# Performance work log

Measured on AMD Instinct MI355X. Metric: run time of the kernel, lower is better.

Reference implementation:

```python
import jax, jax.numpy as jnp
import numpy as np

WET_MIX = 0.3
FEEDBACK = 0.4
ROOM_SIZE = 0.5
NUM_REFL = 8
NUM_HEADS = 4

# Delay kernel table: int(delay) in {0,1,2,>=3} -> kernel_size {identity,3,5,7}.
# A k-tap kernel with padding k//2 == the same kernel zero-padded to 7 taps with padding 3.
def _gauss7(ks):
    g = np.exp(-np.linspace(-2.0, 2.0, ks) ** 2)
    g = g / g.sum()
    out = np.zeros(7, np.float32)
    s = (7 - ks) // 2
    out[s:s + ks] = g
    return out
_delta = np.zeros(7, np.float32); _delta[3] = 1.0
K_TABLE = jnp.asarray(np.stack([_delta, _gauss7(3), _gauss7(5), _gauss7(7)]))  # [4,7]


def _conv2d(x, w, b, pad):
    y = jax.lax.conv_general_dilated(x, w, (1, 1), [(pad, pad), (pad, pad)],
                                     dimension_numbers=('NCHW', 'OIHW', 'NCHW'))
    return y + b[None, :, None, None]


def _delay_line(x, kern7):
    # vertical depthwise Gaussian blur, same for every (batch, channel) plane
    b, c, h, w = x.shape
    k = kern7.reshape(1, 1, 7, 1)
    y = jax.lax.conv_general_dilated(x.reshape(b * c, 1, h, w), k, (1, 1), [(3, 3), (0, 0)],
                                     dimension_numbers=('NCHW', 'OIHW', 'NCHW'))
    return y.reshape(b, c, h, w)


def _forward(x, refl_w, refl_d, sc_w, sc_b, fb_w, fb_b, d1_w, d1_b, d2_w, d2_b,
             in_proj_w, in_proj_b, out_proj_w, out_proj_b, oc_w, oc_b):
    B, C, H, W = x.shape
    scaled = refl_d * ROOM_SIZE
    kidx = jnp.clip(jnp.floor(scaled).astype(jnp.int32), 0, 3)  # int(delay) detaches grad, as in torch

    wet = jnp.zeros_like(x)
    fb_buf = x * 0.1
    spatial = _conv2d(x, sc_w, sc_b, 1)  # [B,2C,H,W]

    for i in range(NUM_REFL):
        refl = _delay_line(fb_buf, K_TABLE[kidx[i]])
        refl = _conv2d(refl, fb_w, fb_b, 1)
        damp = jax.nn.sigmoid(_conv2d(jax.nn.silu(_conv2d(refl, d1_w, d1_b, 0)), d2_w, d2_b, 0))
        refl = refl * damp
        weight = jax.nn.sigmoid(refl_w[i]) * (0.8 ** i)
        wet = wet + refl * weight
        fb_buf = fb_buf + refl * (FEEDBACK * 0.1)

    # MultiheadAttention over L = H*W tokens, embed_dim=C=4, 4 heads (head_dim=1)
    L = H * W
    hd = C // NUM_HEADS
    wet_flat = wet.reshape(B, C, L).transpose(0, 2, 1)           # [B,L,C]
    qkv = wet_flat @ in_proj_w.T + in_proj_b                     # [B,L,3C]
    q, k, v = jnp.split(qkv, 3, axis=-1)
    def heads(t):
        return t.reshape(B, L, NUM_HEADS, hd).transpose(0, 2, 1, 3)  # [B,H,L,hd]
    q, k, v = heads(q), heads(k), heads(v)
    scores = jnp.einsum('bhqd,bhkd->bhqk', q, k) / np.sqrt(hd).astype(np.float32)
    attn = jax.nn.softmax(scores, axis=-1)
    o = jnp.einsum('bhqk,bhkd->bhqd', attn, v)
    o = o.transpose(0, 2, 1, 3).reshape(B, L, C) @ out_proj_w.T + out_proj_b
    wet2 = o.transpose(0, 2, 1).reshape(B, C, H, W)

    combined = jnp.concatenate([spatial, wet2], axis=1)          # [B,3C,H,W]
    processed_wet = _conv2d(combined, oc_w, oc_b, 0)
    return x * (1.0 - WET_MIX) + processed_wet * WET_MIX


def setup_inputs() -> dict:
    key = jax.random.key(0)
    ks = jax.random.split(key, 16)
    B, C, H, W = 2, 4, 64, 64
    f32 = jnp.float32
    return {
        'x': jax.random.normal(ks[0], (B, C, H, W), f32),
        'refl_w': jax.random.normal(ks[1], (8,), f32) * 0.1,
        'refl_d': jax.random.randint(ks[2], (8,), 1, 16).astype(f32),
        'sc_w': jax.random.normal(ks[3], (2 * C, C, 3, 3), f32) * 0.1,
        'sc_b': jnp.zeros((2 * C,), f32),
        'fb_w': jax.random.normal(ks[4], (C, C, 3, 3), f32) * 0.1,
        'fb_b': jnp.zeros((C,), f32),
        'd1_w': jax.random.normal(ks[5], (C // 2, C, 1, 1), f32) * 0.3,
        'd1_b': jnp.zeros((C // 2,), f32),
        'd2_w': jax.random.normal(ks[6], (C, C // 2, 1, 1), f32) * 0.3,
        'd2_b': jnp.zeros((C,), f32),
        'in_proj_w': jax.random.normal(ks[7], (3 * C, C), f32) * 0.3,
        'in_proj_b': jnp.zeros((3 * C,), f32),
        'out_proj_w': jax.random.normal(ks[8], (C, C), f32) * 0.3,
        'out_proj_b': jnp.zeros((C,), f32),
        'oc_w': jax.random.normal(ks[9], (C, 3 * C, 1, 1), f32) * 0.2,
        'oc_b': jnp.zeros((C,), f32),
    }


def reference(x, refl_w, refl_d, sc_w, sc_b, fb_w, fb_b, d1_w, d1_b, d2_w, d2_b,
              in_proj_w, in_proj_b, out_proj_w, out_proj_b, oc_w, oc_b):
    return _forward(x, refl_w, refl_d, sc_w, sc_b, fb_w, fb_b, d1_w, d1_b, d2_w, d2_b,
                    in_proj_w, in_proj_b, out_proj_w, out_proj_b, oc_w, oc_b)
```

## Files before the change

### kernel.cpp

```cpp
#include <hip/hip_runtime.h>
#include <math.h>


#define ZERO4 make_float4(0.f, 0.f, 0.f, 0.f)

__device__ __forceinline__ float sigf(float v) { return 1.0f / (1.0f + __expf(-v)); }

__device__ __forceinline__ float dppL(float v) {
    return __int_as_float(__builtin_amdgcn_mov_dpp(__float_as_int(v), 0x138, 0xf, 0xf, true));
}
__device__ __forceinline__ float dppR(float v) {
    return __int_as_float(__builtin_amdgcn_mov_dpp(__float_as_int(v), 0x130, 0xf, 0xf, true));
}
__device__ __forceinline__ float4 shL4(float4 v) {
    return make_float4(dppL(v.x), dppL(v.y), dppL(v.z), dppL(v.w));
}
__device__ __forceinline__ float4 shR4(float4 v) {
    return make_float4(dppR(v.x), dppR(v.y), dppR(v.z), dppR(v.w));
}

__device__ __forceinline__ void tap(float4& a, const float4 t, const float* wp) {
    a.x += wp[0]   * t.x + wp[9]    * t.y + wp[18]    * t.z + wp[27]    * t.w;
    a.y += wp[36]  * t.x + wp[36+9] * t.y + wp[36+18] * t.z + wp[36+27] * t.w;
    a.z += wp[72]  * t.x + wp[72+9] * t.y + wp[72+18] * t.z + wp[72+27] * t.w;
    a.w += wp[108] * t.x + wp[108+9]* t.y + wp[108+18]* t.z + wp[108+27]* t.w;
}

__global__ __launch_bounds__(1024, 1) void reverb_qkv_kernel(
    const float* __restrict__ x,
    const float* __restrict__ refl_w,
    const float* __restrict__ refl_d,
    const float* __restrict__ fb_w,
    const float* __restrict__ fb_b,
    const float* __restrict__ d1_w,
    const float* __restrict__ d1_b,
    const float* __restrict__ d2_w,
    const float* __restrict__ d2_b,
    const float* __restrict__ ipw,
    const float* __restrict__ ipb,
    float* __restrict__ Qg, float* __restrict__ Kg, float* __restrict__ Vg)
{
    __shared__ float4 P [18 * 64];
    __shared__ float4 BL[18 * 64];
    __shared__ float4 WT[2 * 64];
    __shared__ float  GT[3][8];

    const int blk   = blockIdx.x;
    const int batch = blk >> 5;
    const int own0  = (blk & 31) << 1;
    const int LB    = own0 - 8;
    const int tid   = threadIdx.x;
    const int wy    = tid >> 6;
    const int r     = tid & 63;

    if (tid < 3) {
        const int rr = tid + 1;
        const int ks = 2 * rr + 1;
        const int s  = (7 - ks) >> 1;
        const double step = 4.0 / (double)(ks - 1);
        double g[7]; double sum = 0.0;
        for (int t = 0; t < 7; ++t) {
            if (t < ks) { double u = -2.0 + step * (double)t; g[t] = exp(-u * u); sum += g[t]; }
        }
        for (int t = 0; t < 7; ++t) GT[tid][t] = 0.0f;
        for (int t = 0; t < ks; ++t) GT[tid][s + t] = (float)(g[t] / sum);
    }

    for (int idx = tid; idx < 18 * 64; idx += 1024) {
        const int lc  = idx >> 6;
        const int row = idx & 63;
        const int gc  = LB + lc;
        float4 v = ZERO4;
        if (gc >= 0 && gc < 64) {
            const int base = batch * 16384 + row * 64 + gc;
            v.x = 0.1f * x[base];
            v.y = 0.1f * x[base + 4096];
            v.z = 0.1f * x[base + 8192];
            v.w = 0.1f * x[base + 12288];
        }
        P[idx] = v;
    }
    __syncthreads();

    double w8 = 1.0;
    for (int j = 0; j < 8; ++j) {
        int kidx = (int)floorf(refl_d[j] * 0.5f);
        kidx = kidx < 0 ? 0 : (kidx > 3 ? 3 : kidx);
        float kv[7];
        #pragma unroll
        for (int u = 0; u < 7; ++u) {
            const float dv = (u == 3) ? 1.0f : 0.0f;
            kv[u] = (kidx == 0) ? dv : GT[kidx - 1][u];
        }
        const float wgt = sigf(refl_w[j]) * (float)w8;

        const int clo = max(0, own0 - (7 - j));
        const int chi = min(64, own0 + 2 + (7 - j));

        const int lcA   = (clo - 1) - LB;
        const int nBlur = (chi + 1) - (clo - 1);
        for (int t = wy; t < nBlur; t += 16) {
            const int lc = lcA + t;
            const int gc = LB + lc;
            float4 b = ZERO4;
            if (gc >= 0 && gc < 64) {
                const float4 v  = P[lc * 64 + r];
                const float4 l1 = shL4(v),  l2 = shL4(l1), l3 = shL4(l2);
                const float4 r1 = shR4(v),  r2 = shR4(r1), r3 = shR4(r2);
                b.x = kv[0]*l3.x + kv[1]*l2.x + kv[2]*l1.x + kv[3]*v.x
                    + kv[4]*r1.x + kv[5]*r2.x + kv[6]*r3.x;
                b.y = kv[0]*l3.y + kv[1]*l2.y + kv[2]*l1.y + kv[3]*v.y
                    + kv[4]*r1.y + kv[5]*r2.y + kv[6]*r3.y;
                b.z = kv[0]*l3.z + kv[1]*l2.z + kv[2]*l1.z + kv[3]*v.z
                    + kv[4]*r1.z + kv[5]*r2.z + kv[6]*r3.z;
                b.w = kv[0]*l3.w + kv[1]*l2.w + kv[2]*l1.w + kv[3]*v.w
                    + kv[4]*r1.w + kv[5]*r2.w + kv[6]*r3.w;
            }
            BL[lc * 64 + r] = b;
        }
        __syncthreads();

        const int c = clo + wy;
        if (wy < chi - clo) {
            const int lc = c - LB;
            const float4 bm = BL[(lc - 1) * 64 + r];
            const float4 bc = BL[lc * 64 + r];
            const float4 bp = BL[(lc + 1) * 64 + r];

            float4 acc = make_float4(fb_b[0], fb_b[1], fb_b[2], fb_b[3]);
            tap(acc, shL4(bm), fb_w + 0);  tap(acc, shL4(bc), fb_w + 1);  tap(acc, shL4(bp), fb_w + 2);
            tap(acc, bm,       fb_w + 3);  tap(acc, bc,       fb_w + 4);  tap(acc, bp,       fb_w + 5);
            tap(acc, shR4(bm), fb_w + 6);  tap(acc, shR4(bc), fb_w + 7);  tap(acc, shR4(bp), fb_w + 8);

            float4 rr = acc;
            float h0 = d1_b[0] + d1_w[0]*rr.x + d1_w[1]*rr.y + d1_w[2]*rr.z + d1_w[3]*rr.w;
            float h1 = d1_b[1] + d1_w[4]*rr.x + d1_w[5]*rr.y + d1_w[6]*rr.z + d1_w[7]*rr.w;
            h0 = h0 * sigf(h0);
            h1 = h1 * sigf(h1);
            const float d0  = sigf(d2_b[0] + d2_w[0]*h0 + d2_w[1]*h1);
            const float d1v = sigf(d2_b[1] + d2_w[2]*h0 + d2_w[3]*h1);
            const float d2v = sigf(d2_b[2] + d2_w[4]*h0 + d2_w[5]*h1);
            const float d3v = sigf(d2_b[3] + d2_w[6]*h0 + d2_w[7]*h1);
            rr.x *= d0; rr.y *= d1v; rr.z *= d2v; rr.w *= d3v;

            const float4 oldfb = P[lc * 64 + r];
            P[lc * 64 + r] = make_float4(oldfb.x + 0.04f*rr.x, oldfb.y + 0.04f*rr.y,
                                         oldfb.z + 0.04f*rr.z, oldfb.w + 0.04f*rr.w);

            if (c >= own0 && c < own0 + 2) {
                const int widx = (c - own0) * 64 + r;
                float4 wv = make_float4(wgt*rr.x, wgt*rr.y, wgt*rr.z, wgt*rr.w);
                if (j > 0) {
                    const float4 old = WT[widx];
                    wv.x += old.x; wv.y += old.y; wv.z += old.z; wv.w += old.w;
                }
                WT[widx] = wv;
            }
        }
        __syncthreads();
        w8 *= 0.8;
    }

    if (tid < 128) {
        const int row = tid & 63;
        const int oc  = tid >> 6;
        const int c   = own0 + oc;
        const float4 wv = WT[oc * 64 + row];
        #pragma unroll
        for (int h = 0; h < 4; ++h) {
            const float q = ipb[h]
                + ipw[h*4+0]*wv.x + ipw[h*4+1]*wv.y
                + ipw[h*4+2]*wv.z + ipw[h*4+3]*wv.w;
            const float k = ipb[4+h]
                + ipw[(4+h)*4+0]*wv.x + ipw[(4+h)*4+1]*wv.y
                + ipw[(4+h)*4+2]*wv.z + ipw[(4+h)*4+3]*wv.w;
            const float v = ipb[8+h]
                + ipw[(8+h)*4+0]*wv.x + ipw[(8+h)*4+1]*wv.y
                + ipw[(8+h)*4+2]*wv.z + ipw[(8+h)*4+3]*wv.w;
            const int o = (batch * 4 + h) * 4096 + row * 64 + c;
            Qg[o] = q; Kg[o] = k; Vg[o] = v;
        }
    }
}

__global__ __launch_bounds__(256) void attn_kernel(
    const float* __restrict__ Qg, const float* __restrict__ Kg,
    const float* __restrict__ Vg,
    float* __restrict__ PN, float* __restrict__ PD)
{
    __shared__ float wred[8];
    __shared__ float partN[256], partD[256];

    const int bh  = blockIdx.x >> 8;
    const int sub = (blockIdx.x >> 2) & 63;
    const int ks  = blockIdx.x & 3;
    const int tid = threadIdx.x;

    const float* Kp = Kg + bh * 4096;
    const float* Vp = Vg + bh * 4096;

    float pmax = -3.0e38f, pmin = 3.0e38f;
    for (int t = tid; t < 4096; t += 256) {
        const float kk = Kp[t];
        pmax = fmaxf(pmax, kk);
        pmin = fminf(pmin, kk);
    }
    #pragma unroll
    for (int off = 32; off > 0; off >>= 1) {
        pmax = fmaxf(pmax, __shfl_xor(pmax, off, 64));
        pmin = fminf(pmin, __shfl_xor(pmin, off, 64));
    }
    if ((tid & 63) == 0) { wred[tid >> 6] = pmax; wred[4 + (tid >> 6)] = pmin; }
    __syncthreads();
    const float kmax = fmaxf(fmaxf(wred[0], wred[1]), fmaxf(wred[2], wred[3]));
    const float kmin = fminf(fminf(wred[4], wred[5]), fminf(wred[6], wred[7]));

    const int ql = tid & 63;
    const int kh = __builtin_amdgcn_readfirstlane(tid >> 6);
    const int qi = sub * 64 + ql;

    const float L2E = 1.4426950408889634f;
    const float q  = Qg[bh * 4096 + qi];
    const float q2 = q * L2E;
    const float nm2 = -(((q >= 0.0f) ? q * kmax : q * kmin) * L2E);

    const float4* K4 = (const float4*)Kp;
    const float4* V4 = (const float4*)Vp;
    const int base = ks * 256 + kh * 64;

    float num0 = 0.f, num1 = 0.f, den0 = 0.f, den1 = 0.f;
    #pragma unroll 4
    for (int j = 0; j < 64; j += 2) {
        const float4 ka = K4[base + j];
        const float4 kb = K4[base + j + 1];
        const float4 va = V4[base + j];
        const float4 vb = V4[base + j + 1];
        float e;
        e = __builtin_amdgcn_exp2f(__fmaf_rn(q2, ka.x, nm2)); den0 += e; num0 = __fmaf_rn(e, va.x, num0);
        e = __builtin_amdgcn_exp2f(__fmaf_rn(q2, ka.y, nm2)); den1 += e; num1 = __fmaf_rn(e, va.y, num1);
        e = __builtin_amdgcn_exp2f(__fmaf_rn(q2, ka.z, nm2)); den0 += e; num0 = __fmaf_rn(e, va.z, num0);
        e = __builtin_amdgcn_exp2f(__fmaf_rn(q2, ka.w, nm2)); den1 += e; num1 = __fmaf_rn(e, va.w, num1);
        e = __builtin_amdgcn_exp2f(__fmaf_rn(q2, kb.x, nm2)); den0 += e; num0 = __fmaf_rn(e, vb.x, num0);
        e = __builtin_amdgcn_exp2f(__fmaf_rn(q2, kb.y, nm2)); den1 += e; num1 = __fmaf_rn(e, vb.y, num1);
        e = __builtin_amdgcn_exp2f(__fmaf_rn(q2, kb.z, nm2)); den0 += e; num0 = __fmaf_rn(e, vb.z, num0);
        e = __builtin_amdgcn_exp2f(__fmaf_rn(q2, kb.w, nm2)); den1 += e; num1 = __fmaf_rn(e, vb.w, num1);
    }
    partN[tid] = num0 + num1;
    partD[tid] = den0 + den1;
    __syncthreads();
    if (tid < 64) {
        const float n = partN[tid] + partN[tid + 64] + partN[tid + 128] + partN[tid + 192];
        const float d = partD[tid] + partD[tid + 64] + partD[tid + 128] + partD[tid + 192];
        const int o = bh * 16384 + ks * 4096 + sub * 64 + tid;
        PN[o] = n;
        PD[o] = d;
    }
}

__global__ __launch_bounds__(128) void final_kernel(
    const float* __restrict__ x,
    const float* __restrict__ sc_w, const float* __restrict__ sc_b,
    const float* __restrict__ opw,  const float* __restrict__ opb,
    const float* __restrict__ ocw,  const float* __restrict__ ocb,
    const float* __restrict__ PN,   const float* __restrict__ PD,
    float* __restrict__ out)
{
    const int g   = blockIdx.x * 128 + threadIdx.x;
    const int b   = g >> 12;
    const int pix = g & 4095;
    const int y   = pix >> 6;
    const int xc  = pix & 63;

    float xin[4][3][3];
    #pragma unroll
    for (int ic = 0; ic < 4; ++ic)
        #pragma unroll
        for (int ky = 0; ky < 3; ++ky)
            #pragma unroll
            for (int kx = 0; kx < 3; ++kx) {
                const int yy = y + ky - 1, xx = xc + kx - 1;
                xin[ic][ky][kx] = (yy >= 0 && yy < 64 && xx >= 0 && xx < 64)
                                    ? x[(b * 4 + ic) * 4096 + yy * 64 + xx] : 0.f;
            }

    float sp[8];
    #pragma unroll
    for (int oc = 0; oc < 8; ++oc) {
        float a = sc_b[oc];
        #pragma unroll
        for (int ic = 0; ic < 4; ++ic)
            #pragma unroll
            for (int ky = 0; ky < 3; ++ky)
                #pragma unroll
                for (int kx = 0; kx < 3; ++kx)
                    a += sc_w[(oc * 4 + ic) * 9 + ky * 3 + kx] * xin[ic][ky][kx];
        sp[oc] = a;
    }

    float oh[4];
    #pragma unroll
    for (int h = 0; h < 4; ++h) {
        const int bh = b * 4 + h;
        float n = 0.f, d = 0.f;
        #pragma unroll
        for (int ks = 0; ks < 4; ++ks) {
            n += PN[bh * 16384 + ks * 4096 + pix];
            d += PD[bh * 16384 + ks * 4096 + pix];
        }
        oh[h] = n / d;
    }

    float w2[4];
    #pragma unroll
    for (int c = 0; c < 4; ++c)
        w2[c] = opb[c] + opw[c*4+0]*oh[0] + opw[c*4+1]*oh[1]
                       + opw[c*4+2]*oh[2] + opw[c*4+3]*oh[3];

    #pragma unroll
    for (int c = 0; c < 4; ++c) {
        float a = ocb[c];
        #pragma unroll
        for (int j = 0; j < 8; ++j) a += ocw[c * 12 + j] * sp[j];
        #pragma unroll
        for (int h = 0; h < 4; ++h) a += ocw[c * 12 + 8 + h] * w2[h];
        const int idx = (b * 4 + c) * 4096 + y * 64 + xc;
        out[idx] = 0.7f * x[idx] + 0.3f * a;
    }
}

extern "C" void kernel_launch(void* const* d_in, const int* in_sizes, int n_in,
                              void* d_out, int out_size, void* d_ws, size_t ws_size,
                              hipStream_t stream) {
    const float* x      = (const float*)d_in[0];
    const float* refl_w = (const float*)d_in[1];
    const float* refl_d = (const float*)d_in[2];
    const float* sc_w   = (const float*)d_in[3];
    const float* sc_b   = (const float*)d_in[4];
    const float* fb_w   = (const float*)d_in[5];
    const float* fb_b   = (const float*)d_in[6];
    const float* d1_w   = (const float*)d_in[7];
    const float* d1_b   = (const float*)d_in[8];
    const float* d2_w   = (const float*)d_in[9];
    const float* d2_b   = (const float*)d_in[10];
    const float* ipw    = (const float*)d_in[11];
    const float* ipb    = (const float*)d_in[12];
    const float* opw    = (const float*)d_in[13];
    const float* opb    = (const float*)d_in[14];
    const float* ocw    = (const float*)d_in[15];
    const float* ocb    = (const float*)d_in[16];
    float* out = (float*)d_out;

    float* Q  = (float*)d_ws;
    float* K  = Q + 32768;
    float* V  = K + 32768;
    float* PN = V + 32768;
    float* PD = PN + 131072;

    reverb_qkv_kernel<<<dim3(64), dim3(1024), 0, stream>>>(
        x, refl_w, refl_d, fb_w, fb_b, d1_w, d1_b, d2_w, d2_b, ipw, ipb,
        Q, K, V);
    attn_kernel<<<dim3(2048), dim3(256), 0, stream>>>(Q, K, V, PN, PD);
    final_kernel<<<dim3(64), dim3(128), 0, stream>>>(
        x, sc_w, sc_b, opw, opb, ocw, ocb, PN, PD, out);
}
```

Baseline: 139.5 us.

## Fuse blur into feedback conv with ping-pong buffers; split-K softmax max per chunk

The reverb kernel drops the separate blur pass and its barrier. Each thread now recomputes the vertical blur for its three neighbouring columns from a double-buffered feedback plane, so each reflection needs one sync instead of two, at the cost of computing each blur three times. In the attention kernel, each key split scans only its own 1024 keys for max/min instead of all 4096 and records its own max. The final kernel rescales and combines the partial numerators and denominators log-sum-exp style, which adds a PM workspace buffer and extra exp work.

```diff
diff --git a/kernel.cpp b/kernel.cpp
--- a/kernel.cpp
+++ b/kernel.cpp
@@ -24,6 +24,21 @@
     a.y += wp[36]  * t.x + wp[36+9] * t.y + wp[36+18] * t.z + wp[36+27] * t.w;
     a.z += wp[72]  * t.x + wp[72+9] * t.y + wp[72+18] * t.z + wp[72+27] * t.w;
     a.w += wp[108] * t.x + wp[108+9]* t.y + wp[108+18]* t.z + wp[108+27]* t.w;
+}
+
+__device__ __forceinline__ float4 blur7(float4 v, const float* kv) {
+    const float4 l1 = shL4(v),  l2 = shL4(l1), l3 = shL4(l2);
+    const float4 r1 = shR4(v),  r2 = shR4(r1), r3 = shR4(r2);
+    float4 b;
+    b.x = kv[0]*l3.x + kv[1]*l2.x + kv[2]*l1.x + kv[3]*v.x
+        + kv[4]*r1.x + kv[5]*r2.x + kv[6]*r3.x;
+    b.y = kv[0]*l3.y + kv[1]*l2.y + kv[2]*l1.y + kv[3]*v.y
+        + kv[4]*r1.y + kv[5]*r2.y + kv[6]*r3.y;
+    b.z = kv[0]*l3.z + kv[1]*l2.z + kv[2]*l1.z + kv[3]*v.z
+        + kv[4]*r1.z + kv[5]*r2.z + kv[6]*r3.z;
+    b.w = kv[0]*l3.w + kv[1]*l2.w + kv[2]*l1.w + kv[3]*v.w
+        + kv[4]*r1.w + kv[5]*r2.w + kv[6]*r3.w;
+    return b;
 }
 
 __global__ __launch_bounds__(1024, 1) void reverb_qkv_kernel(
@@ -40,8 +55,8 @@
     const float* __restrict__ ipb,
     float* __restrict__ Qg, float* __restrict__ Kg, float* __restrict__ Vg)
 {
-    __shared__ float4 P [18 * 64];
-    __shared__ float4 BL[18 * 64];
+    __shared__ float4 PA[18 * 64];
+    __shared__ float4 PB[18 * 64];
     __shared__ float4 WT[2 * 64];
     __shared__ float  GT[3][8];
 
@@ -78,12 +93,16 @@
             v.z = 0.1f * x[base + 8192];
             v.w = 0.1f * x[base + 12288];
         }
-        P[idx] = v;
+        PA[idx] = v;
+        PB[idx] = v;
     }
     __syncthreads();
 
     double w8 = 1.0;
     for (int j = 0; j < 8; ++j) {
+        const float4* Pold = (j & 1) ? PB : PA;
+        float4*       Pnew = (j & 1) ? PA : PB;
+
         int kidx = (int)floorf(refl_d[j] * 0.5f);
         kidx = kidx < 0 ? 0 : (kidx > 3 ? 3 : kidx);
         float kv[7];
@@ -97,35 +116,13 @@
         const int clo = max(0, own0 - (7 - j));
         const int chi = min(64, own0 + 2 + (7 - j));
 
-        const int lcA   = (clo - 1) - LB;
-        const int nBlur = (chi + 1) - (clo - 1);
-        for (int t = wy; t < nBlur; t += 16) {
-            const int lc = lcA + t;
-            const int gc = LB + lc;
-            float4 b = ZERO4;
-            if (gc >= 0 && gc < 64) {
-                const float4 v  = P[lc * 64 + r];
-                const float4 l1 = shL4(v),  l2 = shL4(l1), l3 = shL4(l2);
-                const float4 r1 = shR4(v),  r2 = shR4(r1), r3 = shR4(r2);
-                b.x = kv[0]*l3.x + kv[1]*l2.x + kv[2]*l1.x + kv[3]*v.x
-                    + kv[4]*r1.x + kv[5]*r2.x + kv[6]*r3.x;
-                b.y = kv[0]*l3.y + kv[1]*l2.y + kv[2]*l1.y + kv[3]*v.y
-                    + kv[4]*r1.y + kv[5]*r2.y + kv[6]*r3.y;
-                b.z = kv[0]*l3.z + kv[1]*l2.z + kv[2]*l1.z + kv[3]*v.z
-                    + kv[4]*r1.z + kv[5]*r2.z + kv[6]*r3.z;
-                b.w = kv[0]*l3.w + kv[1]*l2.w + kv[2]*l1.w + kv[3]*v.w
-                    + kv[4]*r1.w + kv[5]*r2.w + kv[6]*r3.w;
-            }
-            BL[lc * 64 + r] = b;
-        }
-        __syncthreads();
-
         const int c = clo + wy;
         if (wy < chi - clo) {
             const int lc = c - LB;
-            const float4 bm = BL[(lc - 1) * 64 + r];
-            const float4 bc = BL[lc * 64 + r];
-            const float4 bp = BL[(lc + 1) * 64 + r];
+
+            const float4 bm = (c - 1 >= 0) ? blur7(Pold[(lc - 1) * 64 + r], kv) : ZERO4;
+            const float4 bc = blur7(Pold[lc * 64 + r], kv);
+            const float4 bp = (c + 1 < 64) ? blur7(Pold[(lc + 1) * 64 + r], kv) : ZERO4;
 
             float4 acc = make_float4(fb_b[0], fb_b[1], fb_b[2], fb_b[3]);
             tap(acc, shL4(bm), fb_w + 0);  tap(acc, shL4(bc), fb_w + 1);  tap(acc, shL4(bp), fb_w + 2);
@@ -143,9 +140,11 @@
             const float d3v = sigf(d2_b[3] + d2_w[6]*h0 + d2_w[7]*h1);
             rr.x *= d0; rr.y *= d1v; rr.z *= d2v; rr.w *= d3v;
 
-            const float4 oldfb = P[lc * 64 + r];
-            P[lc * 64 + r] = make_float4(oldfb.x + 0.04f*rr.x, oldfb.y + 0.04f*rr.y,
-                                         oldfb.z + 0.04f*rr.z, oldfb.w + 0.04f*rr.w);
+            if (j < 7) {
+                const float4 oldfb = Pold[lc * 64 + r];
+                Pnew[lc * 64 + r] = make_float4(oldfb.x + 0.04f*rr.x, oldfb.y + 0.04f*rr.y,
+                                                oldfb.z + 0.04f*rr.z, oldfb.w + 0.04f*rr.w);
+            }
 
             if (c >= own0 && c < own0 + 2) {
                 const int widx = (c - own0) * 64 + r;
@@ -186,7 +185,7 @@
 __global__ __launch_bounds__(256) void attn_kernel(
     const float* __restrict__ Qg, const float* __restrict__ Kg,
     const float* __restrict__ Vg,
-    float* __restrict__ PN, float* __restrict__ PD)
+    float* __restrict__ PN, float* __restrict__ PD, float* __restrict__ PM)
 {
     __shared__ float wred[8];
     __shared__ float partN[256], partD[256];
@@ -196,11 +195,12 @@
     const int ks  = blockIdx.x & 3;
     const int tid = threadIdx.x;
 
-    const float* Kp = Kg + bh * 4096;
-    const float* Vp = Vg + bh * 4096;
+    const float* Kp = Kg + bh * 4096 + ks * 1024;
+    const float* Vp = Vg + bh * 4096 + ks * 1024;
 
     float pmax = -3.0e38f, pmin = 3.0e38f;
-    for (int t = tid; t < 4096; t += 256) {
+    #pragma unroll
+    for (int t = tid; t < 1024; t += 256) {
         const float kk = Kp[t];
         pmax = fmaxf(pmax, kk);
         pmin = fminf(pmin, kk);
@@ -222,11 +222,12 @@
     const float L2E = 1.4426950408889634f;
     const float q  = Qg[bh * 4096 + qi];
     const float q2 = q * L2E;
-    const float nm2 = -(((q >= 0.0f) ? q * kmax : q * kmin) * L2E);
+    const float m2 = ((q >= 0.0f) ? q * kmax : q * kmin) * L2E;
+    const float nm2 = -m2;
 
     const float4* K4 = (const float4*)Kp;
     const float4* V4 = (const float4*)Vp;
-    const int base = ks * 256 + kh * 64;
+    const int base = kh * 64;
 
     float num0 = 0.f, num1 = 0.f, den0 = 0.f, den1 = 0.f;
     #pragma unroll 4
@@ -254,6 +255,7 @@
         const int o = bh * 16384 + ks * 4096 + sub * 64 + tid;
         PN[o] = n;
         PD[o] = d;
+        PM[o] = m2;
     }
 }
 
@@ -263,7 +265,7 @@
     const float* __restrict__ opw,  const float* __restrict__ opb,
     const float* __restrict__ ocw,  const float* __restrict__ ocb,
     const float* __restrict__ PN,   const float* __restrict__ PD,
-    float* __restrict__ out)
+    const float* __restrict__ PM,   float* __restrict__ out)
 {
     const int g   = blockIdx.x * 128 + threadIdx.x;
     const int b   = g >> 12;
@@ -301,11 +303,16 @@
     #pragma unroll
     for (int h = 0; h < 4; ++h) {
         const int bh = b * 4 + h;
+        float m2s[4];
+        #pragma unroll
+        for (int ks = 0; ks < 4; ++ks) m2s[ks] = PM[bh * 16384 + ks * 4096 + pix];
+        const float M2 = fmaxf(fmaxf(m2s[0], m2s[1]), fmaxf(m2s[2], m2s[3]));
         float n = 0.f, d = 0.f;
         #pragma unroll
         for (int ks = 0; ks < 4; ++ks) {
-            n += PN[bh * 16384 + ks * 4096 + pix];
-            d += PD[bh * 16384 + ks * 4096 + pix];
+            const float s = __builtin_amdgcn_exp2f(m2s[ks] - M2);
+            n = __fmaf_rn(PN[bh * 16384 + ks * 4096 + pix], s, n);
+            d = __fmaf_rn(PD[bh * 16384 + ks * 4096 + pix], s, d);
         }
         oh[h] = n / d;
     }
@@ -355,11 +362,12 @@
     float* V  = K + 32768;
     float* PN = V + 32768;
     float* PD = PN + 131072;
+    float* PM = PD + 131072;
 
     reverb_qkv_kernel<<<dim3(64), dim3(1024), 0, stream>>>(
         x, refl_w, refl_d, fb_w, fb_b, d1_w, d1_b, d2_w, d2_b, ipw, ipb,
         Q, K, V);
-    attn_kernel<<<dim3(2048), dim3(256), 0, stream>>>(Q, K, V, PN, PD);
+    attn_kernel<<<dim3(2048), dim3(256), 0, stream>>>(Q, K, V, PN, PD, PM);
     final_kernel<<<dim3(64), dim3(128), 0, stream>>>(
-        x, sc_w, sc_b, opw, opb, ocw, ocb, PN, PD, out);
-}
+        x, sc_w, sc_b, opw, opb, ocw, ocb, PN, PD, PM, out);
+}
```

New measurement: 141.6 us. Within noise of the previous version (+1.5%).

## Stage split-local K/V chunk in shared memory and rescale partials by per-split max

Applied to the files above, without the earlier changes.

Each attention block now loads only its own 1024-key chunk of K and V, interleaves them into shared memory as float2 pairs, and computes the max/min of K over that chunk only rather than the full 4096 keys. The inner loop reads one float4 (two key/value pairs) per iteration from LDS instead of separate global K and V loads. Because each split now has its own softmax shift, the kernel writes that shift to a new PM buffer and the final kernel rescales the partial numerators and denominators with exp2 before combining them. This reduces the redundant full-K reduction and the global memory traffic, but adds an extra workspace buffer, extra reads and exp work in the final kernel, and an LDS staging step.

```diff
diff --git a/kernel.cpp b/kernel.cpp
--- a/kernel.cpp
+++ b/kernel.cpp
@@ -186,22 +186,26 @@
 __global__ __launch_bounds__(256) void attn_kernel(
     const float* __restrict__ Qg, const float* __restrict__ Kg,
     const float* __restrict__ Vg,
-    float* __restrict__ PN, float* __restrict__ PD)
+    float* __restrict__ PN, float* __restrict__ PD, float* __restrict__ PM)
 {
-    __shared__ float wred[8];
-    __shared__ float partN[256], partD[256];
+    __shared__ float2 KV[1024];
+    __shared__ float  wred[8];
+    __shared__ float  partN[256], partD[256];
 
     const int bh  = blockIdx.x >> 8;
     const int sub = (blockIdx.x >> 2) & 63;
     const int ks  = blockIdx.x & 3;
     const int tid = threadIdx.x;
 
-    const float* Kp = Kg + bh * 4096;
-    const float* Vp = Vg + bh * 4096;
+    const float* Kp = Kg + bh * 4096 + ks * 1024;
+    const float* Vp = Vg + bh * 4096 + ks * 1024;
 
     float pmax = -3.0e38f, pmin = 3.0e38f;
-    for (int t = tid; t < 4096; t += 256) {
+    #pragma unroll
+    for (int t = tid; t < 1024; t += 256) {
         const float kk = Kp[t];
+        const float vv = Vp[t];
+        KV[t] = make_float2(kk, vv);
         pmax = fmaxf(pmax, kk);
         pmin = fminf(pmin, kk);
     }
@@ -222,28 +226,20 @@
     const float L2E = 1.4426950408889634f;
     const float q  = Qg[bh * 4096 + qi];
     const float q2 = q * L2E;
-    const float nm2 = -(((q >= 0.0f) ? q * kmax : q * kmin) * L2E);
-
-    const float4* K4 = (const float4*)Kp;
-    const float4* V4 = (const float4*)Vp;
-    const int base = ks * 256 + kh * 64;
+    const float m2 = ((q >= 0.0f) ? q * kmax : q * kmin) * L2E;
+    const float nm2 = -m2;
+
+    const float4* KV4 = (const float4*)KV;
+    const int base4 = kh * 128;
 
     float num0 = 0.f, num1 = 0.f, den0 = 0.f, den1 = 0.f;
-    #pragma unroll 4
-    for (int j = 0; j < 64; j += 2) {
-        const float4 ka = K4[base + j];
-        const float4 kb = K4[base + j + 1];
-        const float4 va = V4[base + j];
-        const float4 vb = V4[base + j + 1];
-        float e;
-        e = __builtin_amdgcn_exp2f(__fmaf_rn(q2, ka.x, nm2)); den0 += e; num0 = __fmaf_rn(e, va.x, num0);
-        e = __builtin_amdgcn_exp2f(__fmaf_rn(q2, ka.y, nm2)); den1 += e; num1 = __fmaf_rn(e, va.y, num1);
-        e = __builtin_amdgcn_exp2f(__fmaf_rn(q2, ka.z, nm2)); den0 += e; num0 = __fmaf_rn(e, va.z, num0);
-        e = __builtin_amdgcn_exp2f(__fmaf_rn(q2, ka.w, nm2)); den1 += e; num1 = __fmaf_rn(e, va.w, num1);
-        e = __builtin_amdgcn_exp2f(__fmaf_rn(q2, kb.x, nm2)); den0 += e; num0 = __fmaf_rn(e, vb.x, num0);
-        e = __builtin_amdgcn_exp2f(__fmaf_rn(q2, kb.y, nm2)); den1 += e; num1 = __fmaf_rn(e, vb.y, num1);
-        e = __builtin_amdgcn_exp2f(__fmaf_rn(q2, kb.z, nm2)); den0 += e; num0 = __fmaf_rn(e, vb.z, num0);
-        e = __builtin_amdgcn_exp2f(__fmaf_rn(q2, kb.w, nm2)); den1 += e; num1 = __fmaf_rn(e, vb.w, num1);
+    #pragma unroll 8
+    for (int j = 0; j < 128; ++j) {
+        const float4 f = KV4[base4 + j];
+        const float e0 = __builtin_amdgcn_exp2f(__fmaf_rn(q2, f.x, nm2));
+        den0 += e0;  num0 = __fmaf_rn(e0, f.y, num0);
+        const float e1 = __builtin_amdgcn_exp2f(__fmaf_rn(q2, f.z, nm2));
+        den1 += e1;  num1 = __fmaf_rn(e1, f.w, num1);
     }
     partN[tid] = num0 + num1;
     partD[tid] = den0 + den1;
@@ -254,6 +250,7 @@
         const int o = bh * 16384 + ks * 4096 + sub * 64 + tid;
         PN[o] = n;
         PD[o] = d;
+        PM[o] = m2;
     }
 }
 
@@ -263,7 +260,7 @@
     const float* __restrict__ opw,  const float* __restrict__ opb,
     const float* __restrict__ ocw,  const float* __restrict__ ocb,
     const float* __restrict__ PN,   const float* __restrict__ PD,
-    float* __restrict__ out)
+    const float* __restrict__ PM,   float* __restrict__ out)
 {
     const int g   = blockIdx.x * 128 + threadIdx.x;
     const int b   = g >> 12;
@@ -301,11 +298,16 @@
     #pragma unroll
     for (int h = 0; h < 4; ++h) {
         const int bh = b * 4 + h;
+        float m2s[4];
+        #pragma unroll
+        for (int ks = 0; ks < 4; ++ks) m2s[ks] = PM[bh * 16384 + ks * 4096 + pix];
+        const float M2 = fmaxf(fmaxf(m2s[0], m2s[1]), fmaxf(m2s[2], m2s[3]));
         float n = 0.f, d = 0.f;
         #pragma unroll
         for (int ks = 0; ks < 4; ++ks) {
-            n += PN[bh * 16384 + ks * 4096 + pix];
-            d += PD[bh * 16384 + ks * 4096 + pix];
+            const float s = __builtin_amdgcn_exp2f(m2s[ks] - M2);
+            n = __fmaf_rn(PN[bh * 16384 + ks * 4096 + pix], s, n);
+            d = __fmaf_rn(PD[bh * 16384 + ks * 4096 + pix], s, d);
         }
         oh[h] = n / d;
     }
@@ -355,11 +357,12 @@
     float* V  = K + 32768;
     float* PN = V + 32768;
     float* PD = PN + 131072;
+    float* PM = PD + 131072;
 
     reverb_qkv_kernel<<<dim3(64), dim3(1024), 0, stream>>>(
         x, refl_w, refl_d, fb_w, fb_b, d1_w, d1_b, d2_w, d2_b, ipw, ipb,
         Q, K, V);
-    attn_kernel<<<dim3(2048), dim3(256), 0, stream>>>(Q, K, V, PN, PD);
+    attn_kernel<<<dim3(2048), dim3(256), 0, stream>>>(Q, K, V, PN, PD, PM);
     final_kernel<<<dim3(64), dim3(128), 0, stream>>>(
-        x, sc_w, sc_b, opw, opb, ocw, ocb, PN, PD, out);
-}
+        x, sc_w, sc_b, opw, opb, ocw, ocb, PN, PD, PM, out);
+}
```

After: 136.9 us. About the same (-1.8%).
